# Performance work log

Hardware: AMD Instinct MI355X
Metric: run time of the kernel (lower is better)

The kernel has to match this reference:

```python
import jax, jax.numpy as jnp
import numpy as np
import math

SEQ = 179
EMB = 256
HEADS = 8
EPS = 1e-5


def make_pe(d_model=EMB, max_len=SEQ):
    pos = jnp.arange(max_len, dtype=jnp.float32)[:, None]
    div = jnp.exp(jnp.arange(0, d_model, 2, dtype=jnp.float32) * (-math.log(10000.0) / d_model))
    ang = pos * div * (d_model / max_len)  # [L, d/2]
    pe = jnp.stack([jnp.sin(ang), jnp.cos(ang)], axis=-1).reshape(max_len, d_model)
    return pe  # [L, d]; interleaved sin/cos matches pe[:,0::2]=sin, pe[:,1::2]=cos


def make_spec_wghts(n=SEQ):
    idx = jnp.arange(n, dtype=jnp.float32)
    return jnp.abs(idx[None, :] - idx[:, None]) / n  # [S, S]


def layernorm(x, g, b):
    mu = jnp.mean(x, axis=-1, keepdims=True)
    var = jnp.mean(jnp.square(x - mu), axis=-1, keepdims=True)
    return (x - mu) * jax.lax.rsqrt(var + EPS) * g + b


def attention(x, wq, wk, wv, g, b, sw):
    B, S, E = x.shape
    D = E // HEADS
    scale = E ** (-0.5)  # note: full emb_size, matching the original
    q = (x @ wq.T).reshape(B, S, HEADS, D)
    k = (x @ wk.T).reshape(B, S, HEADS, D)
    v = (x @ wv.T).reshape(B, S, HEADS, D)
    attn = jnp.einsum('bshd,bthd->bhst', q, k) * scale
    attn = attn * sw  # elementwise distance weighting (zeroes the diagonal)
    attn = jax.nn.softmax(attn, axis=-1)
    out = jnp.einsum('bhst,bthd->bshd', attn, v).reshape(B, S, E)
    return layernorm(out, g, b)


def setup_inputs() -> dict:
    key = jax.random.key(0)
    ks = jax.random.split(key, 10)
    s = 0.02
    return {
        'x': jax.random.normal(ks[0], (512, 1, 720), jnp.float32),
        'conv_w': jax.random.normal(ks[1], (EMB, 1, 8), jnp.float32) * s,
        'conv_b': jnp.zeros((EMB,), jnp.float32),
        'bn_g': jnp.ones((EMB,), jnp.float32),
        'bn_b': jnp.zeros((EMB,), jnp.float32),
        'bn_mean': jnp.zeros((EMB,), jnp.float32),
        'bn_var': jnp.ones((EMB,), jnp.float32),
        'wq1': jax.random.normal(ks[2], (EMB, EMB), jnp.float32) * s,
        'wk1': jax.random.normal(ks[3], (EMB, EMB), jnp.float32) * s,
        'wv1': jax.random.normal(ks[4], (EMB, EMB), jnp.float32) * s,
        'lnA1_g': jnp.ones((EMB,), jnp.float32),
        'lnA1_b': jnp.zeros((EMB,), jnp.float32),
        'wq2': jax.random.normal(ks[5], (EMB, EMB), jnp.float32) * s,
        'wk2': jax.random.normal(ks[6], (EMB, EMB), jnp.float32) * s,
        'wv2': jax.random.normal(ks[7], (EMB, EMB), jnp.float32) * s,
        'lnA2_g': jnp.ones((EMB,), jnp.float32),
        'lnA2_b': jnp.zeros((EMB,), jnp.float32),
        'ln2_g': jnp.ones((EMB,), jnp.float32),
        'ln2_b': jnp.zeros((EMB,), jnp.float32),
        'out_w': jax.random.normal(ks[8], (10, EMB), jnp.float32) * s,
        'out_b': jnp.zeros((10,), jnp.float32),
    }


def reference(x, conv_w, conv_b, bn_g, bn_b, bn_mean, bn_var,
              wq1, wk1, wv1, lnA1_g, lnA1_b,
              wq2, wk2, wv2, lnA2_g, lnA2_b,
              ln2_g, ln2_b, out_w, out_b):
    pe = make_pe()
    sw = make_spec_wghts()
    # conv embed: [B,1,720] -> [B,EMB,179]
    h = jax.lax.conv_general_dilated(x, conv_w, window_strides=(4,), padding='VALID',
                                     dimension_numbers=('NCH', 'OIH', 'NCH'))
    h = h + conv_b[None, :, None]
    # BatchNorm1d (inference) + ReLU
    inv = jax.lax.rsqrt(bn_var + EPS)
    h = (h - bn_mean[None, :, None]) * (bn_g * inv)[None, :, None] + bn_b[None, :, None]
    h = jax.nn.relu(h)
    x_src = jnp.transpose(h, (0, 2, 1))  # [B, 179, EMB]
    x1 = x_src + pe
    att = attention(x1, wq1, wk1, wv1, lnA1_g, lnA1_b, sw)
    x2 = att + pe
    att = attention(x2, wq2, wk2, wv2, lnA2_g, lnA2_b, sw)
    att = layernorm(att, ln2_g, ln2_b)
    pooled = jnp.mean(att, axis=1)  # GAP over seq: [B, EMB]
    return pooled @ out_w.T + out_b  # [B, num_classes]
```

## Files before the change

kernel.cpp:

```cpp
#include <hip/hip_runtime.h>
#include <hip/hip_bf16.h>
#include <math.h>

#define B_TOT 512
#define SEQ   179
#define EMB   256
#define HEADS 8
#define HD    32
#define LIN   720
#define EPSV  1e-5f

typedef __attribute__((ext_vector_type(8))) short bf16x8;
typedef __attribute__((ext_vector_type(4))) float f32x4;

__device__ __forceinline__ short f2bf(float f) {
    unsigned u = __float_as_uint(f);
    return (short)((u + 0x7fff + ((u >> 16) & 1)) >> 16);
}
__device__ __forceinline__ unsigned cvt_pk_bf16(float lo, float hi) {
    unsigned r;
    asm("v_cvt_pk_bf16_f32 %0, %1, %2" : "=v"(r) : "v"(lo), "v"(hi));
    return r;
}

__global__ void pe_kernel(float* __restrict__ pe) {
    int idx = blockIdx.x * 256 + threadIdx.x;
    if (idx >= SEQ * EMB) return;
    int s = idx / EMB, e = idx % EMB;
    int i = e >> 1;
    float dv  = expf((float)(2 * i) * (-9.210340371976184f / (float)EMB));
    float ang = (float)s * dv * ((float)EMB / (float)SEQ);
    pe[idx] = (e & 1) ? cosf(ang) : sinf(ang);
}

__global__ void fold_conv_kernel(const float* __restrict__ cw, const float* __restrict__ cb,
                                 const float* __restrict__ g, const float* __restrict__ bb,
                                 const float* __restrict__ mean, const float* __restrict__ var,
                                 float* __restrict__ wt, float* __restrict__ bp) {
    int e = threadIdx.x;
    float is = g[e] * rsqrtf(var[e] + EPSV);
#pragma unroll
    for (int j = 0; j < 8; ++j) wt[j * EMB + e] = cw[e * 8 + j] * is;
    bp[e] = (cb[e] - mean[e]) * is + bb[e];
}

__global__ void cvt6_kernel(const float* __restrict__ s0, const float* __restrict__ s1,
                            const float* __restrict__ s2, const float* __restrict__ s3,
                            const float* __restrict__ s4, const float* __restrict__ s5,
                            __hip_bfloat16* __restrict__ dst, int n) {
    int w = blockIdx.y;
    const float* src = (w == 0) ? s0 : (w == 1) ? s1 : (w == 2) ? s2
                     : (w == 3) ? s3 : (w == 4) ? s4 : s5;
    __hip_bfloat16* d = dst + (size_t)w * n;
    int i = (blockIdx.x * 256 + threadIdx.x) * 4;
    if (i < n) {
        float4 v = *reinterpret_cast<const float4*>(&src[i]);
        d[i + 0] = __float2bfloat16(v.x);
        d[i + 1] = __float2bfloat16(v.y);
        d[i + 2] = __float2bfloat16(v.z);
        d[i + 3] = __float2bfloat16(v.w);
    }
}

__global__ __launch_bounds__(256) void embed_kernel(
    const float* __restrict__ x, const float* __restrict__ wt,
    const float* __restrict__ bp, const float* __restrict__ pe,
    __hip_bfloat16* __restrict__ Xb, int M)
{
    int lane = threadIdx.x & 63;
    int wv   = threadIdx.x >> 6;
    int e0   = lane * 4;

    float wreg[8][4];
#pragma unroll
    for (int j = 0; j < 8; ++j)
        *reinterpret_cast<float4*>(wreg[j]) = *reinterpret_cast<const float4*>(&wt[j * EMB + e0]);
    float4 bpv = *reinterpret_cast<const float4*>(&bp[e0]);

    int r0 = blockIdx.x * 16 + wv * 4;
#pragma unroll
    for (int rr = 0; rr < 4; ++rr) {
        int r = r0 + rr;
        if (r >= M) return;
        int b = r / SEQ, s = r - b * SEQ;
        const float* xr = &x[(size_t)b * LIN + s * 4];
        float4 xa = *reinterpret_cast<const float4*>(xr);
        float4 xc = *reinterpret_cast<const float4*>(xr + 4);
        float xi[8] = {xa.x, xa.y, xa.z, xa.w, xc.x, xc.y, xc.z, xc.w};
        float4 pv = *reinterpret_cast<const float4*>(&pe[s * EMB + e0]);
        const float* bpa = reinterpret_cast<const float*>(&bpv);
        const float* pva = reinterpret_cast<const float*>(&pv);
        float y[4];
#pragma unroll
        for (int c = 0; c < 4; ++c) {
            float acc = bpa[c];
#pragma unroll
            for (int j = 0; j < 8; ++j) acc += xi[j] * wreg[j][c];
            y[c] = fmaxf(acc, 0.f) + pva[c];
        }
        uint2 o;
        o.x = cvt_pk_bf16(y[0], y[1]);
        o.y = cvt_pk_bf16(y[2], y[3]);
        *reinterpret_cast<uint2*>(&Xb[(size_t)r * EMB + e0]) = o;
    }
}

__global__ __launch_bounds__(256) void gemm_qkv_mfma(
    const __hip_bfloat16* __restrict__ A,
    const __hip_bfloat16* __restrict__ Wset,
    __hip_bfloat16* __restrict__ Q, __hip_bfloat16* __restrict__ K,
    __hip_bfloat16* __restrict__ V, int M)
{
    int by = blockIdx.y;
    int wsel = by >> 1;
    const __hip_bfloat16* W = Wset + (size_t)wsel * EMB * EMB;
    __hip_bfloat16* C = (wsel == 0) ? Q : (wsel == 1 ? K : V);
    int nbase = (by & 1) * 128;
    int mbase = blockIdx.x * 128;

    __shared__ __hip_bfloat16 As[128][64];
    __shared__ __hip_bfloat16 Bs[128][64];

    int tid  = threadIdx.x;
    int wave = tid >> 6, lane = tid & 63;
    int wr = wave >> 1, wc = wave & 1;

    int r0   = tid >> 3;
    int srcs = (tid & 7) ^ (r0 & 7);
    const __hip_bfloat16* gA = A + (size_t)(mbase + r0) * EMB + srcs * 8;
    const __hip_bfloat16* gB = W + (size_t)(nbase + r0) * EMB + srcs * 8;

    f32x4 acc[4][4];
#pragma unroll
    for (int i = 0; i < 4; ++i)
#pragma unroll
        for (int j = 0; j < 4; ++j) acc[i][j] = (f32x4){0.f, 0.f, 0.f, 0.f};

    for (int kt = 0; kt < EMB; kt += 64) {
        if (kt) __syncthreads();
#pragma unroll
        for (int i = 0; i < 4; ++i) {
            __hip_bfloat16* l = &As[0][0] + i * 2048 + tid * 8;
            __builtin_amdgcn_global_load_lds(
                (const __attribute__((address_space(1))) void*)(gA + (size_t)i * 32 * EMB + kt),
                (__attribute__((address_space(3))) void*)l, 16, 0, 0);
        }
#pragma unroll
        for (int i = 0; i < 4; ++i) {
            __hip_bfloat16* l = &Bs[0][0] + i * 2048 + tid * 8;
            __builtin_amdgcn_global_load_lds(
                (const __attribute__((address_space(1))) void*)(gB + (size_t)i * 32 * EMB + kt),
                (__attribute__((address_space(3))) void*)l, 16, 0, 0);
        }
        asm volatile("s_waitcnt vmcnt(0)" ::: "memory");
        __syncthreads();

#pragma unroll
        for (int kk = 0; kk < 2; ++kk) {
            bf16x8 af[4], bfr[4];
            int sg = kk * 4 + (lane >> 4);
#pragma unroll
            for (int mi = 0; mi < 4; ++mi) {
                int row = wr * 64 + mi * 16 + (lane & 15);
                int sl  = sg ^ (row & 7);
                af[mi] = *reinterpret_cast<const bf16x8*>(&As[row][sl * 8]);
            }
#pragma unroll
            for (int ni = 0; ni < 4; ++ni) {
                int row = wc * 64 + ni * 16 + (lane & 15);
                int sl  = sg ^ (row & 7);
                bfr[ni] = *reinterpret_cast<const bf16x8*>(&Bs[row][sl * 8]);
            }
#pragma unroll
            for (int mi = 0; mi < 4; ++mi)
#pragma unroll
                for (int ni = 0; ni < 4; ++ni)
                    acc[mi][ni] = __builtin_amdgcn_mfma_f32_16x16x32_bf16(
                        af[mi], bfr[ni], acc[mi][ni], 0, 0, 0);
        }
    }

    int rg = lane >> 4, cli = lane & 15;
#pragma unroll
    for (int mi = 0; mi < 4; ++mi)
#pragma unroll
        for (int j = 0; j < 4; ++j) {
            int m = mbase + wr * 64 + mi * 16 + rg * 4 + j;
            if (m < M) {
#pragma unroll
                for (int ni = 0; ni < 4; ++ni)
                    C[(size_t)m * EMB + nbase + wc * 64 + ni * 16 + cli] =
                        __float2bfloat16(acc[mi][ni][j]);
            }
        }
}

__global__ __launch_bounds__(256) void attn_mfma_kernel(
    const __hip_bfloat16* __restrict__ Qb, const __hip_bfloat16* __restrict__ Kb,
    const __hip_bfloat16* __restrict__ Vb, __hip_bfloat16* __restrict__ O)
{
    int bh = blockIdx.x;
    int b = bh >> 3, h = bh & 7;
    const size_t base = (size_t)b * SEQ * EMB + (size_t)h * HD;

    __shared__ short K2[96][64];
    __shared__ short Vt[32][208];

    int tid  = threadIdx.x;
    int wave = tid >> 6, lane = tid & 63;
    int cl = lane & 15, rg = lane >> 4;

    for (int u = tid; u < 192 * 4; u += 256) {
        int t = u >> 2, d0 = (u & 3) << 3;
        uint4 kv = make_uint4(0, 0, 0, 0);
        if (t < SEQ) kv = *reinterpret_cast<const uint4*>(&Kb[base + (size_t)t * EMB + d0]);
        int krow = t >> 1;
        int kphy = (((t & 1) * 4 + (d0 >> 3)) ^ (krow & 7));
        *reinterpret_cast<uint4*>(&K2[krow][kphy * 8]) = kv;
    }
    if (tid < 192) {
        int tq = tid >> 2, d0 = (tid & 3) << 3;
        int t0 = tq * 4;
        uint4 r0 = make_uint4(0,0,0,0), r1 = r0, r2 = r0, r3 = r0;
        if (t0 + 0 < SEQ) r0 = *reinterpret_cast<const uint4*>(&Vb[base + (size_t)(t0+0)*EMB + d0]);
        if (t0 + 1 < SEQ) r1 = *reinterpret_cast<const uint4*>(&Vb[base + (size_t)(t0+1)*EMB + d0]);
        if (t0 + 2 < SEQ) r2 = *reinterpret_cast<const uint4*>(&Vb[base + (size_t)(t0+2)*EMB + d0]);
        if (t0 + 3 < SEQ) r3 = *reinterpret_cast<const uint4*>(&Vb[base + (size_t)(t0+3)*EMB + d0]);
        const unsigned* q0 = reinterpret_cast<const unsigned*>(&r0);
        const unsigned* q1 = reinterpret_cast<const unsigned*>(&r1);
        const unsigned* q2 = reinterpret_cast<const unsigned*>(&r2);
        const unsigned* q3 = reinterpret_cast<const unsigned*>(&r3);
#pragma unroll
        for (int k = 0; k < 8; ++k) {
            int dw = k >> 1, sh = (k & 1) * 16;
            unsigned a0 = (q0[dw] >> sh) & 0xffffu;
            unsigned a1 = (q1[dw] >> sh) & 0xffffu;
            unsigned a2 = (q2[dw] >> sh) & 0xffffu;
            unsigned a3 = (q3[dw] >> sh) & 0xffffu;
            uint2 w;
            w.x = a0 | (a1 << 16);
            w.y = a2 | (a3 << 16);
            *reinterpret_cast<uint2*>(&Vt[d0 + k][t0]) = w;
        }
    }
    __syncthreads();

    const float csw2 = (0.0625f / (float)SEQ) * 1.4426950408889634f;
    int srcA4 = ((((rg & 1) << 5) + cl) << 2);
    int srcB4 = srcA4 + 64;
    bool hi2  = (rg >= 2);

    for (int qt = 0; qt < 3; ++qt) {
        int qbase = wave * 48 + qt * 16;
        int sq = qbase + cl;
        bf16x8 aq = {};
        if (sq < SEQ)
            aq = *reinterpret_cast<const bf16x8*>(&Qb[base + (size_t)sq * EMB + rg * 8]);
        float sf = (float)sq;

        f32x4 olo = {0.f, 0.f, 0.f, 0.f}, ohi = {0.f, 0.f, 0.f, 0.f};
        float lrow = 0.f;

#pragma unroll
        for (int blk = 0; blk < 6; ++blk) {
            f32x4 s1, s2;
            {
                int t = blk * 32 + cl;
                int kr = t >> 1;
                int kph = (((t & 1) * 4 + rg) ^ (kr & 7));
                bf16x8 kf = *reinterpret_cast<const bf16x8*>(&K2[kr][kph * 8]);
                s1 = __builtin_amdgcn_mfma_f32_16x16x32_bf16(
                    kf, aq, (f32x4){0.f, 0.f, 0.f, 0.f}, 0, 0, 0);
            }
            {
                int t = blk * 32 + 16 + cl;
                int kr = t >> 1;
                int kph = (((t & 1) * 4 + rg) ^ (kr & 7));
                bf16x8 kf = *reinterpret_cast<const bf16x8*>(&K2[kr][kph * 8]);
                s2 = __builtin_amdgcn_mfma_f32_16x16x32_bf16(
                    kf, aq, (f32x4){0.f, 0.f, 0.f, 0.f}, 0, 0, 0);
            }

            int tb1 = blk * 32 + rg * 4;
            int tb2 = tb1 + 16;
            float p1[4], p2[4];
#pragma unroll
            for (int j = 0; j < 4; ++j) {
                p1[j] = exp2f(s1[j] * (fabsf(sf - (float)(tb1 + j)) * csw2));
                p2[j] = exp2f(s2[j] * (fabsf(sf - (float)(tb2 + j)) * csw2));
            }
            if (blk == 5) {
#pragma unroll
                for (int j = 0; j < 4; ++j)
                    if (tb2 + j >= SEQ) p2[j] = 0.f;
            }
            lrow += (p1[0] + p1[1]) + (p1[2] + p1[3])
                  + (p2[0] + p2[1]) + (p2[2] + p2[3]);

            int w10 = (int)cvt_pk_bf16(p1[0], p1[1]);
            int w11 = (int)cvt_pk_bf16(p1[2], p1[3]);
            int w20 = (int)cvt_pk_bf16(p2[0], p2[1]);
            int w21 = (int)cvt_pk_bf16(p2[2], p2[3]);
            int d0a = __builtin_amdgcn_ds_bpermute(srcA4, w10);
            int d0b = __builtin_amdgcn_ds_bpermute(srcA4, w20);
            int d1a = __builtin_amdgcn_ds_bpermute(srcA4, w11);
            int d1b = __builtin_amdgcn_ds_bpermute(srcA4, w21);
            int d2a = __builtin_amdgcn_ds_bpermute(srcB4, w10);
            int d2b = __builtin_amdgcn_ds_bpermute(srcB4, w20);
            int d3a = __builtin_amdgcn_ds_bpermute(srcB4, w11);
            int d3b = __builtin_amdgcn_ds_bpermute(srcB4, w21);
            uint4 pw;
            pw.x = (unsigned)(hi2 ? d0b : d0a);
            pw.y = (unsigned)(hi2 ? d1b : d1a);
            pw.z = (unsigned)(hi2 ? d2b : d2a);
            pw.w = (unsigned)(hi2 ? d3b : d3a);
            bf16x8 pfrag = *reinterpret_cast<bf16x8*>(&pw);

            bf16x8 vlo = *reinterpret_cast<const bf16x8*>(&Vt[cl][blk * 32 + rg * 8]);
            bf16x8 vhi = *reinterpret_cast<const bf16x8*>(&Vt[cl + 16][blk * 32 + rg * 8]);
            olo = __builtin_amdgcn_mfma_f32_16x16x32_bf16(vlo, pfrag, olo, 0, 0, 0);
            ohi = __builtin_amdgcn_mfma_f32_16x16x32_bf16(vhi, pfrag, ohi, 0, 0, 0);
        }

        lrow += __shfl_xor(lrow, 16);
        lrow += __shfl_xor(lrow, 32);

        if (sq < SEQ) {
            float rl = 1.0f / lrow;
            __hip_bfloat16* op = &O[base + (size_t)sq * EMB];
            uint2 wlo, whi;
            wlo.x = cvt_pk_bf16(olo[0] * rl, olo[1] * rl);
            wlo.y = cvt_pk_bf16(olo[2] * rl, olo[3] * rl);
            whi.x = cvt_pk_bf16(ohi[0] * rl, ohi[1] * rl);
            whi.y = cvt_pk_bf16(ohi[2] * rl, ohi[3] * rl);
            *reinterpret_cast<uint2*>(&op[rg * 4])      = wlo;
            *reinterpret_cast<uint2*>(&op[16 + rg * 4]) = whi;
        }
    }
}

__global__ __launch_bounds__(256) void ln_pe4_kernel(
    const __hip_bfloat16* __restrict__ X, const float* __restrict__ g,
    const float* __restrict__ bb, const float* __restrict__ pe,
    __hip_bfloat16* __restrict__ Xb, int M)
{
    int r = blockIdx.x * 4 + (threadIdx.x >> 6);
    if (r >= M) return;
    int lane = threadIdx.x & 63;
    int s = r % SEQ;
    int c0 = lane * 4;

    uint2 raw = *reinterpret_cast<const uint2*>(&X[(size_t)r * EMB + c0]);
    float v[4];
    v[0] = __uint_as_float((raw.x & 0xffffu) << 16);
    v[1] = __uint_as_float(raw.x & 0xffff0000u);
    v[2] = __uint_as_float((raw.y & 0xffffu) << 16);
    v[3] = __uint_as_float(raw.y & 0xffff0000u);

    float sum = v[0] + v[1] + v[2] + v[3];
    float sq  = v[0]*v[0] + v[1]*v[1] + v[2]*v[2] + v[3]*v[3];
#pragma unroll
    for (int off = 32; off > 0; off >>= 1) {
        sum += __shfl_xor(sum, off);
        sq  += __shfl_xor(sq,  off);
    }
    float mu  = sum * (1.0f / EMB);
    float var = sq * (1.0f / EMB) - mu * mu;
    float is  = rsqrtf(var + EPSV);

    float4 gv = *reinterpret_cast<const float4*>(&g[c0]);
    float4 bv = *reinterpret_cast<const float4*>(&bb[c0]);
    float4 pv = *reinterpret_cast<const float4*>(&pe[s * EMB + c0]);
    float y0 = (v[0] - mu) * is * gv.x + bv.x + pv.x;
    float y1 = (v[1] - mu) * is * gv.y + bv.y + pv.y;
    float y2 = (v[2] - mu) * is * gv.z + bv.z + pv.z;
    float y3 = (v[3] - mu) * is * gv.w + bv.w + pv.w;

    uint2 o;
    o.x = cvt_pk_bf16(y0, y1);
    o.y = cvt_pk_bf16(y2, y3);
    *reinterpret_cast<uint2*>(&Xb[(size_t)r * EMB + c0]) = o;
}

__global__ __launch_bounds__(512) void lnfc_kernel(
    const __hip_bfloat16* __restrict__ X,
    const float* __restrict__ g1, const float* __restrict__ b1,
    const float* __restrict__ g2, const float* __restrict__ b2,
    const float* __restrict__ ow, const float* __restrict__ ob,
    float* __restrict__ out)
{
    int b    = blockIdx.x;
    int tid  = threadIdx.x;
    int wave = tid >> 6, lane = tid & 63;

    float g1v[4], b1v[4], g2v[4], b2v[4], pooled[4];
#pragma unroll
    for (int j = 0; j < 4; ++j) {
        int c = lane + 64 * j;
        g1v[j] = g1[c]; b1v[j] = b1[c];
        g2v[j] = g2[c]; b2v[j] = b2[c];
        pooled[j] = 0.f;
    }

    for (int s = wave; s < SEQ; s += 8) {
        const __hip_bfloat16* row = &X[((size_t)b * SEQ + s) * EMB];
        float v[4];
#pragma unroll
        for (int j = 0; j < 4; ++j) v[j] = __bfloat162float(row[lane + 64 * j]);

        float sum = v[0] + v[1] + v[2] + v[3];
        float sq  = v[0]*v[0] + v[1]*v[1] + v[2]*v[2] + v[3]*v[3];
#pragma unroll
        for (int off = 32; off > 0; off >>= 1) {
            sum += __shfl_xor(sum, off);
            sq  += __shfl_xor(sq,  off);
        }
        float mu  = sum * (1.0f / EMB);
        float var = sq * (1.0f / EMB) - mu * mu;
        float is  = rsqrtf(var + EPSV);
        float y[4];
#pragma unroll
        for (int j = 0; j < 4; ++j) y[j] = (v[j] - mu) * is * g1v[j] + b1v[j];

        sum = y[0] + y[1] + y[2] + y[3];
        sq  = y[0]*y[0] + y[1]*y[1] + y[2]*y[2] + y[3]*y[3];
#pragma unroll
        for (int off = 32; off > 0; off >>= 1) {
            sum += __shfl_xor(sum, off);
            sq  += __shfl_xor(sq,  off);
        }
        mu  = sum * (1.0f / EMB);
        var = sq * (1.0f / EMB) - mu * mu;
        is  = rsqrtf(var + EPSV);
#pragma unroll
        for (int j = 0; j < 4; ++j) pooled[j] += (y[j] - mu) * is * g2v[j] + b2v[j];
    }

    __shared__ float pp[8][EMB];
#pragma unroll
    for (int j = 0; j < 4; ++j) pp[wave][lane + 64 * j] = pooled[j];
    __syncthreads();
    __shared__ float pool[EMB];
    if (tid < EMB) {
        float pl = 0.f;
#pragma unroll
        for (int w = 0; w < 8; ++w) pl += pp[w][tid];
        pool[tid] = pl * (1.0f / (float)SEQ);
    }
    __syncthreads();
    if (tid < 10) {
        float o = ob[tid];
        for (int k = 0; k < EMB; ++k) o += pool[k] * ow[tid * EMB + k];
        out[b * 10 + tid] = o;
    }
}

extern "C" void kernel_launch(void* const* d_in, const int* in_sizes, int n_in,
                              void* d_out, int out_size, void* d_ws, size_t ws_size,
                              hipStream_t stream)
{
    const float* x      = (const float*)d_in[0];
    const float* conv_w = (const float*)d_in[1];
    const float* conv_b = (const float*)d_in[2];
    const float* bn_g   = (const float*)d_in[3];
    const float* bn_b   = (const float*)d_in[4];
    const float* bn_m   = (const float*)d_in[5];
    const float* bn_v   = (const float*)d_in[6];
    const float* wq1    = (const float*)d_in[7];
    const float* wk1    = (const float*)d_in[8];
    const float* wv1    = (const float*)d_in[9];
    const float* lnA1_g = (const float*)d_in[10];
    const float* lnA1_b = (const float*)d_in[11];
    const float* wq2    = (const float*)d_in[12];
    const float* wk2    = (const float*)d_in[13];
    const float* wv2    = (const float*)d_in[14];
    const float* lnA2_g = (const float*)d_in[15];
    const float* lnA2_b = (const float*)d_in[16];
    const float* ln2_g  = (const float*)d_in[17];
    const float* ln2_b  = (const float*)d_in[18];
    const float* out_w  = (const float*)d_in[19];
    const float* out_b  = (const float*)d_in[20];
    float* out = (float*)d_out;

    const size_t peN = (size_t)SEQ * EMB;
    const size_t wN  = (size_t)EMB * EMB;
    const size_t foldN = 8 * EMB + EMB;

    int chunk = B_TOT;
    while (chunk > 1) {
        size_t M    = (size_t)chunk * SEQ;
        size_t Mpad = (M + 127) / 128 * 128;
        size_t need = (peN + foldN) * 4 + 6 * wN * 2 + (Mpad + 4 * M) * EMB * 2;
        if (need <= ws_size) break;
        chunk >>= 1;
    }
    size_t M    = (size_t)chunk * SEQ;
    size_t Mpad = (M + 127) / 128 * 128;

    float*          pe = (float*)d_ws;
    float*          wt = pe + peN;
    float*          bp = wt + 8 * EMB;
    __hip_bfloat16* Wb = (__hip_bfloat16*)(bp + EMB);
    __hip_bfloat16* Xb = Wb + 6 * wN;
    __hip_bfloat16* Ob = Xb + Mpad * EMB;
    __hip_bfloat16* Qb = Ob + M * EMB;
    __hip_bfloat16* Kb = Qb + M * EMB;
    __hip_bfloat16* Vb = Kb + M * EMB;

    pe_kernel<<<(SEQ * EMB + 255) / 256, 256, 0, stream>>>(pe);
    fold_conv_kernel<<<1, 256, 0, stream>>>(conv_w, conv_b, bn_g, bn_b, bn_m, bn_v, wt, bp);
    {
        dim3 cg((unsigned)(wN / 1024), 6);
        cvt6_kernel<<<cg, 256, 0, stream>>>(wq1, wk1, wv1, wq2, wk2, wv2, Wb, (int)wN);
    }

    for (int b0 = 0; b0 < B_TOT; b0 += chunk) {
        int Bc = chunk;
        int Mi = Bc * SEQ;
        dim3 ggrid((unsigned)(Mpad / 128), 6);

        embed_kernel<<<(Mi + 15) / 16, 256, 0, stream>>>(
            x + (size_t)b0 * LIN, wt, bp, pe, Xb, Mi);

        gemm_qkv_mfma<<<ggrid, 256, 0, stream>>>(Xb, Wb, Qb, Kb, Vb, Mi);
        attn_mfma_kernel<<<Bc * HEADS, 256, 0, stream>>>(Qb, Kb, Vb, Ob);
        ln_pe4_kernel<<<(Mi + 3) / 4, 256, 0, stream>>>(Ob, lnA1_g, lnA1_b, pe, Xb, Mi);

        gemm_qkv_mfma<<<ggrid, 256, 0, stream>>>(Xb, Wb + 3 * wN, Qb, Kb, Vb, Mi);
        attn_mfma_kernel<<<Bc * HEADS, 256, 0, stream>>>(Qb, Kb, Vb, Ob);
        lnfc_kernel<<<Bc, 512, 0, stream>>>(Ob, lnA2_g, lnA2_b, ln2_g, ln2_b,
                                            out_w, out_b, out + (size_t)b0 * 10);
    }
}
```

Baseline: 360.7 us.

## Use 16x16x16 MFMA for PV to drop bpermute shuffles; reorder GEMM grid

The attention PV product now feeds the softmax probabilities straight into two 16x16x16 bf16 MFMAs per half. The score accumulator layout already matches the B-operand layout of that instruction, so the eight ds_bpermute cross-lane shuffles and selects per block go away. In exchange it issues twice as many smaller MFMA instructions and does more narrow LDS reads of V, with the V^T row padded to 212 to reduce bank conflicts. The QKV GEMM grid is also swapped so consecutive blocks share the same M tile across the six weight tiles, which should improve L2 reuse of activations.

```diff
diff --git a/kernel.cpp b/kernel.cpp
--- a/kernel.cpp
+++ b/kernel.cpp
@@ -11,16 +11,23 @@
 #define EPSV  1e-5f
 
 typedef __attribute__((ext_vector_type(8))) short bf16x8;
+typedef __attribute__((ext_vector_type(4))) short bf16x4;
 typedef __attribute__((ext_vector_type(4))) float f32x4;
 
-__device__ __forceinline__ short f2bf(float f) {
-    unsigned u = __float_as_uint(f);
-    return (short)((u + 0x7fff + ((u >> 16) & 1)) >> 16);
-}
 __device__ __forceinline__ unsigned cvt_pk_bf16(float lo, float hi) {
     unsigned r;
     asm("v_cvt_pk_bf16_f32 %0, %1, %2" : "=v"(r) : "v"(lo), "v"(hi));
     return r;
+}
+
+__device__ __forceinline__ f32x4 mfma16x16x16(bf16x4 a, bf16x4 b, f32x4 c) {
+#if __has_builtin(__builtin_amdgcn_mfma_f32_16x16x16bf16_1k)
+    return __builtin_amdgcn_mfma_f32_16x16x16bf16_1k(a, b, c, 0, 0, 0);
+#else
+    asm volatile("v_mfma_f32_16x16x16_bf16 %0, %1, %2, %0"
+                 : "+v"(c) : "v"(a), "v"(b));
+    return c;
+#endif
 }
 
 __global__ void pe_kernel(float* __restrict__ pe) {
@@ -111,12 +118,12 @@
     __hip_bfloat16* __restrict__ Q, __hip_bfloat16* __restrict__ K,
     __hip_bfloat16* __restrict__ V, int M)
 {
-    int by = blockIdx.y;
+    int by = blockIdx.x;
     int wsel = by >> 1;
     const __hip_bfloat16* W = Wset + (size_t)wsel * EMB * EMB;
     __hip_bfloat16* C = (wsel == 0) ? Q : (wsel == 1 ? K : V);
     int nbase = (by & 1) * 128;
-    int mbase = blockIdx.x * 128;
+    int mbase = blockIdx.y * 128;
 
     __shared__ __hip_bfloat16 As[128][64];
     __shared__ __hip_bfloat16 Bs[128][64];
@@ -204,7 +211,7 @@
     const size_t base = (size_t)b * SEQ * EMB + (size_t)h * HD;
 
     __shared__ short K2[96][64];
-    __shared__ short Vt[32][208];
+    __shared__ short Vt[32][212];
 
     int tid  = threadIdx.x;
     int wave = tid >> 6, lane = tid & 63;
@@ -246,9 +253,6 @@
     __syncthreads();
 
     const float csw2 = (0.0625f / (float)SEQ) * 1.4426950408889634f;
-    int srcA4 = ((((rg & 1) << 5) + cl) << 2);
-    int srcB4 = srcA4 + 64;
-    bool hi2  = (rg >= 2);
 
     for (int qt = 0; qt < 3; ++qt) {
         int qbase = wave * 48 + qt * 16;
@@ -297,29 +301,23 @@
             lrow += (p1[0] + p1[1]) + (p1[2] + p1[3])
                   + (p2[0] + p2[1]) + (p2[2] + p2[3]);
 
-            int w10 = (int)cvt_pk_bf16(p1[0], p1[1]);
-            int w11 = (int)cvt_pk_bf16(p1[2], p1[3]);
-            int w20 = (int)cvt_pk_bf16(p2[0], p2[1]);
-            int w21 = (int)cvt_pk_bf16(p2[2], p2[3]);
-            int d0a = __builtin_amdgcn_ds_bpermute(srcA4, w10);
-            int d0b = __builtin_amdgcn_ds_bpermute(srcA4, w20);
-            int d1a = __builtin_amdgcn_ds_bpermute(srcA4, w11);
-            int d1b = __builtin_amdgcn_ds_bpermute(srcA4, w21);
-            int d2a = __builtin_amdgcn_ds_bpermute(srcB4, w10);
-            int d2b = __builtin_amdgcn_ds_bpermute(srcB4, w20);
-            int d3a = __builtin_amdgcn_ds_bpermute(srcB4, w11);
-            int d3b = __builtin_amdgcn_ds_bpermute(srcB4, w21);
-            uint4 pw;
-            pw.x = (unsigned)(hi2 ? d0b : d0a);
-            pw.y = (unsigned)(hi2 ? d1b : d1a);
-            pw.z = (unsigned)(hi2 ? d2b : d2a);
-            pw.w = (unsigned)(hi2 ? d3b : d3a);
-            bf16x8 pfrag = *reinterpret_cast<bf16x8*>(&pw);
-
-            bf16x8 vlo = *reinterpret_cast<const bf16x8*>(&Vt[cl][blk * 32 + rg * 8]);
-            bf16x8 vhi = *reinterpret_cast<const bf16x8*>(&Vt[cl + 16][blk * 32 + rg * 8]);
-            olo = __builtin_amdgcn_mfma_f32_16x16x32_bf16(vlo, pfrag, olo, 0, 0, 0);
-            ohi = __builtin_amdgcn_mfma_f32_16x16x32_bf16(vhi, pfrag, ohi, 0, 0, 0);
+            uint2 u1, u2;
+            u1.x = cvt_pk_bf16(p1[0], p1[1]);
+            u1.y = cvt_pk_bf16(p1[2], p1[3]);
+            u2.x = cvt_pk_bf16(p2[0], p2[1]);
+            u2.y = cvt_pk_bf16(p2[2], p2[3]);
+            bf16x4 pf1 = *reinterpret_cast<bf16x4*>(&u1);
+            bf16x4 pf2 = *reinterpret_cast<bf16x4*>(&u2);
+
+            int tA = blk * 32 + rg * 4;
+            bf16x4 v1lo = *reinterpret_cast<const bf16x4*>(&Vt[cl][tA]);
+            bf16x4 v2lo = *reinterpret_cast<const bf16x4*>(&Vt[cl][tA + 16]);
+            bf16x4 v1hi = *reinterpret_cast<const bf16x4*>(&Vt[cl + 16][tA]);
+            bf16x4 v2hi = *reinterpret_cast<const bf16x4*>(&Vt[cl + 16][tA + 16]);
+            olo = mfma16x16x16(v1lo, pf1, olo);
+            olo = mfma16x16x16(v2lo, pf2, olo);
+            ohi = mfma16x16x16(v1hi, pf1, ohi);
+            ohi = mfma16x16x16(v2hi, pf2, ohi);
         }
 
         lrow += __shfl_xor(lrow, 16);
@@ -517,7 +515,7 @@
     for (int b0 = 0; b0 < B_TOT; b0 += chunk) {
         int Bc = chunk;
         int Mi = Bc * SEQ;
-        dim3 ggrid((unsigned)(Mpad / 128), 6);
+        dim3 ggrid(6, (unsigned)(Mpad / 128));
 
         embed_kernel<<<(Mi + 15) / 16, 256, 0, stream>>>(
             x + (size_t)b0 * LIN, wt, bp, pe, Xb, Mi);
```

Measured after the change: 344.4 us. 1.05x faster.
